# Optimization experiments

Hardware: AMD Instinct MI355X
Metric: run time of the kernel (lower is better)

The kernel has to match this reference:

```python
import jax, jax.numpy as jnp
import numpy as np

D_MODEL = 1024
N_HEADS = 16
HEAD_DIM = D_MODEL // N_HEADS
D_FF = 4096
B, T = 2, 2048


def layernorm(x, g, b, eps=1e-5):
    mu = jnp.mean(x, axis=-1, keepdims=True)
    var = jnp.var(x, axis=-1, keepdims=True)
    return (x - mu) * jax.lax.rsqrt(var + eps) * g + b


def setup_inputs() -> dict:
    key = jax.random.key(0)
    ks = jax.random.split(key, 8)
    s = 0.02
    return {
        "x": jax.random.normal(ks[0], (B, T, D_MODEL), dtype=jnp.float32),
        "ln1_g": jnp.ones((D_MODEL,), jnp.float32),
        "ln1_b": jnp.zeros((D_MODEL,), jnp.float32),
        "qkv_w": jax.random.normal(ks[1], (D_MODEL, 3 * D_MODEL), jnp.float32) * s,
        "qkv_b": jnp.zeros((3 * D_MODEL,), jnp.float32),
        "proj_w": jax.random.normal(ks[2], (D_MODEL, D_MODEL), jnp.float32) * s,
        "proj_b": jnp.zeros((D_MODEL,), jnp.float32),
        "ln2_g": jnp.ones((D_MODEL,), jnp.float32),
        "ln2_b": jnp.zeros((D_MODEL,), jnp.float32),
        "mlp_w1": jax.random.normal(ks[3], (D_MODEL, D_FF), jnp.float32) * s,
        "mlp_b1": jnp.zeros((D_FF,), jnp.float32),
        "mlp_w2": jax.random.normal(ks[4], (D_FF, D_MODEL), jnp.float32) * s,
        "mlp_b2": jnp.zeros((D_MODEL,), jnp.float32),
    }


def reference(x, ln1_g, ln1_b, qkv_w, qkv_b, proj_w, proj_b,
              ln2_g, ln2_b, mlp_w1, mlp_b1, mlp_w2, mlp_b2):
    Bv, Tv, C = x.shape
    scale = HEAD_DIM ** -0.5
    # --- attention branch ---
    h = layernorm(x, ln1_g, ln1_b)
    qkv = h @ qkv_w + qkv_b                                   # [B,T,3C]
    qkv = qkv.reshape(Bv, Tv, 3, N_HEADS, HEAD_DIM)
    q, k, v = qkv[:, :, 0], qkv[:, :, 1], qkv[:, :, 2]        # [B,T,H,Dh]
    att = jnp.einsum('bqhd,bkhd->bhqk', q, k) * scale         # [B,H,T,T]
    causal = jnp.tril(jnp.ones((Tv, Tv), dtype=bool))
    att = jnp.where(causal[None, None], att, -jnp.inf)
    att = jax.nn.softmax(att, axis=-1)
    out = jnp.einsum('bhqk,bkhd->bqhd', att, v).reshape(Bv, Tv, C)
    out = out @ proj_w + proj_b
    x = x + out
    # --- mlp branch ---
    h2 = layernorm(x, ln2_g, ln2_b)
    h2 = jax.nn.gelu(h2 @ mlp_w1 + mlp_b1, approximate=False)
    x = x + (h2 @ mlp_w2 + mlp_b2)
    return x
```

## Files before the change

kernel.cpp:

```cpp
#include <hip/hip_runtime.h>
#include <hip/hip_bf16.h>
#include <cstdint>

typedef __attribute__((ext_vector_type(4))) float f32x4;
typedef __attribute__((ext_vector_type(16))) float f32x16;
typedef __attribute__((ext_vector_type(8))) __bf16 bf16x8;
typedef __attribute__((ext_vector_type(4))) __bf16 bf16x4;
typedef __attribute__((ext_vector_type(4))) uint32_t u32x4;
typedef __attribute__((ext_vector_type(2))) unsigned int u32x2;

#define EPI_BF16 0
#define EPI_GELU 1
#define EPI_RES  2
#define EPI_PART 3

__device__ __forceinline__ void gll16(const void* g, void* l) {
  __builtin_amdgcn_global_load_lds((__attribute__((address_space(1))) void*)(g),
                                   (__attribute__((address_space(3))) void*)(l), 16, 0, 0);
}

__global__ __launch_bounds__(256)
void convT(const float* __restrict__ W, __bf16* __restrict__ WT, int Kd, int Nd)
{
  __shared__ __bf16 t[64][72];
  const int tid = threadIdx.x;
  const int n0 = blockIdx.x * 64, k0 = blockIdx.y * 64;
#pragma unroll
  for (int i = 0; i < 4; ++i) {
    const int c = i * 256 + tid;
    const int r = c >> 4, cc = (c & 15) * 4;
    const float4 v = *(const float4*)(W + (size_t)(k0 + r) * Nd + n0 + cc);
    bf16x4 tv; tv[0] = (__bf16)v.x; tv[1] = (__bf16)v.y; tv[2] = (__bf16)v.z; tv[3] = (__bf16)v.w;
    *(bf16x4*)&t[r][cc] = tv;
  }
  __syncthreads();
#pragma unroll
  for (int i = 0; i < 2; ++i) {
    const int c = i * 256 + tid;
    const int n = c >> 3, s = (c & 7) * 8;
    bf16x8 o;
#pragma unroll
    for (int j = 0; j < 8; ++j) o[j] = t[s + j][n];
    *(bf16x8*)(WT + (size_t)(n0 + n) * Kd + k0 + s) = o;
  }
}

__global__ __launch_bounds__(256)
void ln_rows(const float* __restrict__ x, const float* __restrict__ g,
             const float* __restrict__ b, __bf16* __restrict__ out)
{
  const int row = blockIdx.x;
  const int tid = threadIdx.x;
  const float4 v = *(const float4*)(x + (size_t)row * 1024 + tid * 4);
  float s = v.x + v.y + v.z + v.w;
  float q = v.x * v.x + v.y * v.y + v.z * v.z + v.w * v.w;
#pragma unroll
  for (int o = 32; o; o >>= 1) { s += __shfl_xor(s, o); q += __shfl_xor(q, o); }
  __shared__ float red[8];
  const int wid = tid >> 6;
  if ((tid & 63) == 0) { red[wid] = s; red[4 + wid] = q; }
  __syncthreads();
  s = red[0] + red[1] + red[2] + red[3];
  q = red[4] + red[5] + red[6] + red[7];
  const float mu = s * (1.0f / 1024.0f);
  const float var = q * (1.0f / 1024.0f) - mu * mu;
  const float rs = rsqrtf(var + 1e-5f);
  bf16x4 o4;
#pragma unroll
  for (int i = 0; i < 4; ++i) {
    const int c = tid * 4 + i;
    const float xv = (&v.x)[i];
    o4[i] = (__bf16)((xv - mu) * rs * g[c] + b[c]);
  }
  *(bf16x4*)(out + (size_t)row * 1024 + tid * 4) = o4;
}

template<int EPI>
__global__ __launch_bounds__(256)
void gemm_bt(const __bf16* __restrict__ A, const __bf16* __restrict__ BT,
             const float* __restrict__ bias, const float* __restrict__ R,
             void* __restrict__ Out, int M, int N, int K)
{
  const int tid = threadIdx.x;
  const int lane = tid & 63, wid = tid >> 6;
  const int l15 = lane & 15, lg = lane >> 4;
  const int wm = (wid >> 1) * 64, wn = (wid & 1) * 64;
  const int nwg = gridDim.x * gridDim.y;
  const int hw = blockIdx.y * gridDim.x + blockIdx.x;
  const int logical = (hw & 7) * (nwg >> 3) + (hw >> 3);
  const int rowBase = (logical / gridDim.x) * 128;
  const int colBase = (logical % gridDim.x) * 128;
  const int kLen = K / gridDim.z;
  const int kBeg = blockIdx.z * kLen;
  __shared__ __bf16 As[128 * 32];
  __shared__ __bf16 Bs[128 * 32];
  f32x4 acc[4][4] = {};
  const int fsw = ((l15 >> 1) & 3) << 3;

  for (int k0 = kBeg; k0 < kBeg + kLen; k0 += 32) {
#pragma unroll
    for (int i = 0; i < 2; ++i) {
      const int c = i * 256 + tid;
      const int r = c >> 2;
      const int s = ((c & 3) ^ ((r >> 1) & 3)) * 8;
      gll16(A + (size_t)(rowBase + r) * K + (k0 + s), As + c * 8);
    }
#pragma unroll
    for (int i = 0; i < 2; ++i) {
      const int c = i * 256 + tid;
      const int r = c >> 2;
      const int s = ((c & 3) ^ ((r >> 1) & 3)) * 8;
      gll16(BT + (size_t)(colBase + r) * K + (k0 + s), Bs + c * 8);
    }
    __syncthreads();
    bf16x8 af[4], bfr[4];
#pragma unroll
    for (int m = 0; m < 4; ++m) af[m] = *(const bf16x8*)(As + (wm + m * 16 + l15) * 32 + (lg * 8 ^ fsw));
#pragma unroll
    for (int n = 0; n < 4; ++n) bfr[n] = *(const bf16x8*)(Bs + (wn + n * 16 + l15) * 32 + (lg * 8 ^ fsw));
#pragma unroll
    for (int m = 0; m < 4; ++m)
#pragma unroll
      for (int n = 0; n < 4; ++n)
        acc[m][n] = __builtin_amdgcn_mfma_f32_16x16x32_bf16(af[m], bfr[n], acc[m][n], 0, 0, 0);
    __syncthreads();
  }
#pragma unroll
  for (int m = 0; m < 4; ++m) {
#pragma unroll
    for (int n = 0; n < 4; ++n) {
      const int col = colBase + wn + n * 16 + l15;
      float bb = 0.0f;
      if constexpr (EPI != EPI_PART) bb = bias[col];
#pragma unroll
      for (int i = 0; i < 4; ++i) {
        const int row = rowBase + wm + m * 16 + lg * 4 + i;
        float v = acc[m][n][i] + bb;
        if constexpr (EPI == EPI_GELU) {
          v = 0.5f * v * (1.0f + erff(v * 0.70710678118654752f));
          ((__bf16*)Out)[(size_t)row * N + col] = (__bf16)v;
        } else if constexpr (EPI == EPI_BF16) {
          ((__bf16*)Out)[(size_t)row * N + col] = (__bf16)v;
        } else if constexpr (EPI == EPI_RES) {
          v += R[(size_t)row * N + col];
          ((float*)Out)[(size_t)row * N + col] = v;
        } else {
          ((float*)Out)[((size_t)blockIdx.z * M + row) * N + col] = v;
        }
      }
    }
  }
}

__global__ __launch_bounds__(256)
void reduce2(const float* __restrict__ P, const float* __restrict__ bias,
             const float* __restrict__ R, float* __restrict__ Out, int MN, int N)
{
  const size_t e = ((size_t)blockIdx.x * 256 + threadIdx.x) * 4;
  const float4 a = *(const float4*)(P + e);
  const float4 b = *(const float4*)(P + (size_t)MN + e);
  const float4 r = *(const float4*)(R + e);
  const float4 bb = *(const float4*)(bias + (e & (size_t)(N - 1)));
  float4 o;
  o.x = a.x + b.x + r.x + bb.x;
  o.y = a.y + b.y + r.y + bb.y;
  o.z = a.z + b.z + r.z + bb.z;
  o.w = a.w + b.w + r.w + bb.w;
  *(float4*)(Out + e) = o;
}

__global__ __launch_bounds__(256)
void rearrange(const __bf16* __restrict__ qkv, __bf16* __restrict__ Q,
               __bf16* __restrict__ Kb, __bf16* __restrict__ VT)
{
  __shared__ __bf16 vt[64][72];
  const int tid = threadIdx.x;
  const int bid = blockIdx.x;
  const int bh = bid >> 5, tt = bid & 31;
  const int b = bh >> 4, h = bh & 15;
  const int t0 = tt * 64;
#pragma unroll
  for (int i = 0; i < 2; ++i) {
    const int c = i * 256 + tid;
    const int tk = c >> 3, d0 = (c & 7) * 8;
    const size_t srow = (size_t)(b * 2048 + t0 + tk) * 3072 + h * 64 + d0;
    const size_t drow = (size_t)(bh * 2048 + t0 + tk) * 64 + d0;
    *(bf16x8*)(Q + drow) = *(const bf16x8*)(qkv + srow);
    *(bf16x8*)(Kb + drow) = *(const bf16x8*)(qkv + srow + 1024);
    *(bf16x8*)&vt[tk][d0] = *(const bf16x8*)(qkv + srow + 2048);
  }
  __syncthreads();
#pragma unroll
  for (int i = 0; i < 2; ++i) {
    const int c = i * 256 + tid;
    const int d = c >> 3, s = (c & 7) * 8;
    bf16x8 o;
#pragma unroll
    for (int j = 0; j < 8; ++j) o[j] = vt[s + j][d];
    *(bf16x8*)(VT + (size_t)(bh * 64 + d) * 2048 + t0 + s) = o;
  }
}

__global__ __launch_bounds__(128)
void attn(const __bf16* __restrict__ Q, const __bf16* __restrict__ K,
          const __bf16* __restrict__ VT, __bf16* __restrict__ O)
{
  const int bid = blockIdx.x;
  const int bh = bid >> 5, qt = 31 - (bid & 31);
  const int tid = threadIdx.x;
  const int lane = tid & 63, w = tid >> 6;
  const int l31 = lane & 31, hi = lane >> 5;
  __shared__ __bf16 Ks[64 * 64];
  __shared__ __bf16 Vs[64 * 64];
  const size_t base = (size_t)bh * 2048 * 64;
  const int qrow0 = qt * 64 + w * 32;
  const int xsw = (l31 & 7) << 3;

  bf16x8 qf[4];
#pragma unroll
  for (int s = 0; s < 4; ++s)
    qf[s] = *(const bf16x8*)(Q + base + (size_t)(qrow0 + l31) * 64 + s * 16 + hi * 8);

  f32x16 oa0 = {}, oa1 = {};
  float mst = -INFINITY, lst = 0.0f;

  for (int j = 0; j <= qt; ++j) {
#pragma unroll
    for (int rnd = 0; rnd < 4; ++rnd) {
      const int c = rnd * 128 + tid;
      const int r = c >> 3;
      const int e = ((c & 7) ^ (r & 7)) * 8;
      gll16(K + base + (size_t)(j * 64 + r) * 64 + e, Ks + c * 8);
      gll16(VT + base + (size_t)r * 2048 + j * 64 + e, Vs + c * 8);
    }
    __syncthreads();

    f32x16 s0v = {}, s1v = {};
#pragma unroll
    for (int s = 0; s < 4; ++s) {
      const int co = (s * 16 + hi * 8) ^ xsw;
      bf16x8 ak0 = *(const bf16x8*)(Ks + l31 * 64 + co);
      bf16x8 ak1 = *(const bf16x8*)(Ks + (32 + l31) * 64 + co);
      s0v = __builtin_amdgcn_mfma_f32_32x32x16_bf16(ak0, qf[s], s0v, 0, 0, 0);
      s1v = __builtin_amdgcn_mfma_f32_32x32x16_bf16(ak1, qf[s], s1v, 0, 0, 0);
    }
#pragma unroll
    for (int rg = 0; rg < 16; ++rg) { s0v[rg] *= 0.125f; s1v[rg] *= 0.125f; }
    if (j == qt) {
      const int qg = qrow0 + l31;
#pragma unroll
      for (int rg = 0; rg < 16; ++rg) {
        const int kr = j * 64 + ((rg & 3) + 8 * (rg >> 2)) + 4 * hi;
        if (kr > qg) s0v[rg] = -INFINITY;
        if (kr + 32 > qg) s1v[rg] = -INFINITY;
      }
    }
    float mx = s0v[0];
#pragma unroll
    for (int rg = 1; rg < 16; ++rg) mx = fmaxf(mx, s0v[rg]);
#pragma unroll
    for (int rg = 0; rg < 16; ++rg) mx = fmaxf(mx, s1v[rg]);
    mx = fmaxf(mx, __shfl_xor(mx, 32));
    const float mnew = fmaxf(mst, mx);
    const float cf = __expf(mst - mnew);
    float rs = 0.0f;
#pragma unroll
    for (int rg = 0; rg < 16; ++rg) {
      s0v[rg] = __expf(s0v[rg] - mnew); rs += s0v[rg];
      s1v[rg] = __expf(s1v[rg] - mnew); rs += s1v[rg];
    }
    rs += __shfl_xor(rs, 32);
    lst = lst * cf + rs;
    mst = mnew;
#pragma unroll
    for (int rg = 0; rg < 16; ++rg) {
      const float cb = __shfl(cf, (rg & 3) + 8 * (rg >> 2) + 4 * hi);
      oa0[rg] *= cb; oa1[rg] *= cb;
    }
#pragma unroll
    for (int s = 0; s < 4; ++s) {
      const int br = (s & 1) * 8;
      uint32_t wA0, wA1, wB0, wB1;
      if (s < 2) {
        asm("v_cvt_pk_bf16_f32 %0, %1, %2" : "=v"(wA0) : "v"(s0v[br + 0]), "v"(s0v[br + 1]));
        asm("v_cvt_pk_bf16_f32 %0, %1, %2" : "=v"(wA1) : "v"(s0v[br + 2]), "v"(s0v[br + 3]));
        asm("v_cvt_pk_bf16_f32 %0, %1, %2" : "=v"(wB0) : "v"(s0v[br + 4]), "v"(s0v[br + 5]));
        asm("v_cvt_pk_bf16_f32 %0, %1, %2" : "=v"(wB1) : "v"(s0v[br + 6]), "v"(s0v[br + 7]));
      } else {
        asm("v_cvt_pk_bf16_f32 %0, %1, %2" : "=v"(wA0) : "v"(s1v[br + 0]), "v"(s1v[br + 1]));
        asm("v_cvt_pk_bf16_f32 %0, %1, %2" : "=v"(wA1) : "v"(s1v[br + 2]), "v"(s1v[br + 3]));
        asm("v_cvt_pk_bf16_f32 %0, %1, %2" : "=v"(wB0) : "v"(s1v[br + 4]), "v"(s1v[br + 5]));
        asm("v_cvt_pk_bf16_f32 %0, %1, %2" : "=v"(wB1) : "v"(s1v[br + 6]), "v"(s1v[br + 7]));
      }
      const u32x2 r0 = __builtin_amdgcn_permlane32_swap(wA0, wB0, false, false);
      const u32x2 r1 = __builtin_amdgcn_permlane32_swap(wA1, wB1, false, false);
      u32x4 uu; uu.x = r0.x; uu.y = r1.x; uu.z = r0.y; uu.w = r1.y;
      const bf16x8 pa = __builtin_bit_cast(bf16x8, uu);
      const int co = (s * 16 + hi * 8) ^ xsw;
      bf16x8 bv0 = *(const bf16x8*)(Vs + l31 * 64 + co);
      bf16x8 bv1 = *(const bf16x8*)(Vs + (32 + l31) * 64 + co);
      oa0 = __builtin_amdgcn_mfma_f32_32x32x16_bf16(pa, bv0, oa0, 0, 0, 0);
      oa1 = __builtin_amdgcn_mfma_f32_32x32x16_bf16(pa, bv1, oa1, 0, 0, 0);
    }
    __syncthreads();
  }
  const float inv = 1.0f / lst;
  const int b = bh >> 4, hd = bh & 15;
#pragma unroll
  for (int rg = 0; rg < 16; ++rg) {
    const int cr = (rg & 3) + 8 * (rg >> 2) + 4 * hi;
    const float ib = __shfl(inv, cr);
    const int qr = qrow0 + cr;
    O[(size_t)(b * 2048 + qr) * 1024 + hd * 64 + l31]      = (__bf16)(oa0[rg] * ib);
    O[(size_t)(b * 2048 + qr) * 1024 + hd * 64 + 32 + l31] = (__bf16)(oa1[rg] * ib);
  }
}

extern "C" void kernel_launch(void* const* d_in, const int* in_sizes, int n_in,
                              void* d_out, int out_size, void* d_ws, size_t ws_size,
                              hipStream_t stream)
{
  const float* x      = (const float*)d_in[0];
  const float* ln1_g  = (const float*)d_in[1];
  const float* ln1_b  = (const float*)d_in[2];
  const float* qkv_w  = (const float*)d_in[3];
  const float* qkv_b  = (const float*)d_in[4];
  const float* proj_w = (const float*)d_in[5];
  const float* proj_b = (const float*)d_in[6];
  const float* ln2_g  = (const float*)d_in[7];
  const float* ln2_b  = (const float*)d_in[8];
  const float* mlp_w1 = (const float*)d_in[9];
  const float* mlp_b1 = (const float*)d_in[10];
  const float* mlp_w2 = (const float*)d_in[11];
  const float* mlp_b2 = (const float*)d_in[12];

  char* ws = (char*)d_ws;
  __bf16* qkvT  = (__bf16*)(ws + 0);
  __bf16* projT = (__bf16*)(ws + 6291456);
  __bf16* w1T   = (__bf16*)(ws + 8388608);
  __bf16* w2T   = (__bf16*)(ws + 16777216);
  float*  x2    = (float*) (ws + 25165824);
  __bf16* act1  = (__bf16*)(ws + 41943040);
  __bf16* h1    = (__bf16*)(ws + 41943040);
  __bf16* qkv   = (__bf16*)(ws + 50331648);
  float*  part  = (float*) (ws + 75497472);
  __bf16* h2    = (__bf16*)(ws + 75497472);
  __bf16* Qb    = (__bf16*)(ws + 75497472);
  __bf16* Kb    = (__bf16*)(ws + 83886080);
  __bf16* VTb   = (__bf16*)(ws + 92274688);
  __bf16* attO  = (__bf16*)(ws + 100663296);

  convT<<<dim3(48, 16), 256, 0, stream>>>(qkv_w, qkvT, 1024, 3072);
  convT<<<dim3(16, 16), 256, 0, stream>>>(proj_w, projT, 1024, 1024);
  convT<<<dim3(64, 16), 256, 0, stream>>>(mlp_w1, w1T, 1024, 4096);
  convT<<<dim3(16, 64), 256, 0, stream>>>(mlp_w2, w2T, 4096, 1024);

  ln_rows<<<4096, 256, 0, stream>>>(x, ln1_g, ln1_b, h1);
  gemm_bt<EPI_BF16><<<dim3(24, 32), 256, 0, stream>>>(h1, qkvT, qkv_b, nullptr, qkv, 4096, 3072, 1024);
  rearrange<<<1024, 256, 0, stream>>>(qkv, Qb, Kb, VTb);
  attn<<<1024, 128, 0, stream>>>(Qb, Kb, VTb, attO);
  gemm_bt<EPI_RES><<<dim3(8, 32), 256, 0, stream>>>(attO, projT, proj_b, x, x2, 4096, 1024, 1024);
  ln_rows<<<4096, 256, 0, stream>>>(x2, ln2_g, ln2_b, h2);
  gemm_bt<EPI_GELU><<<dim3(32, 32), 256, 0, stream>>>(h2, w1T, mlp_b1, nullptr, act1, 4096, 4096, 1024);
  gemm_bt<EPI_PART><<<dim3(8, 32, 2), 256, 0, stream>>>(act1, w2T, nullptr, nullptr, part, 4096, 1024, 4096);
  reduce2<<<4096, 256, 0, stream>>>(part, mlp_b2, x2, (float*)d_out, 4096 * 1024, 1024);
}
```

Measured before the change: 417.6 us.

## Merge weight conversions, split-K proj GEMM, 4-way bf16 split-K for MLP down-proj

Fuses the four weight transpose/convert launches into one kernel that dispatches on block index. The attention output projection becomes a 2-way split-K GEMM with a separate reduce that adds bias and residual. The MLP down-projection moves from 2-way fp32 partials to 4-way bf16 partials reduced by a new kernel. The aim is more blocks in flight for the small-N GEMMs (256 blocks before) and fewer launches, at the cost of extra partial-sum traffic, extra reduce launches, and bf16 rounding of the partial sums.

```diff
diff --git a/kernel.cpp b/kernel.cpp
--- a/kernel.cpp
+++ b/kernel.cpp
@@ -9,10 +9,11 @@
 typedef __attribute__((ext_vector_type(4))) uint32_t u32x4;
 typedef __attribute__((ext_vector_type(2))) unsigned int u32x2;
 
-#define EPI_BF16 0
-#define EPI_GELU 1
-#define EPI_RES  2
-#define EPI_PART 3
+#define EPI_BF16  0
+#define EPI_GELU  1
+#define EPI_RES   2
+#define EPI_PART  3
+#define EPI_PARTB 4
 
 __device__ __forceinline__ void gll16(const void* g, void* l) {
   __builtin_amdgcn_global_load_lds((__attribute__((address_space(1))) void*)(g),
@@ -20,11 +21,20 @@
 }
 
 __global__ __launch_bounds__(256)
-void convT(const float* __restrict__ W, __bf16* __restrict__ WT, int Kd, int Nd)
+void convT_all(const float* __restrict__ W0, __bf16* __restrict__ T0,
+               const float* __restrict__ W1, __bf16* __restrict__ T1,
+               const float* __restrict__ W2, __bf16* __restrict__ T2,
+               const float* __restrict__ W3, __bf16* __restrict__ T3)
 {
   __shared__ __bf16 t[64][72];
+  const int bid = blockIdx.x;
+  const float* W; __bf16* WT; int Kd, Nd, nx, lb;
+  if (bid < 768)       { W = W0; WT = T0; Kd = 1024; Nd = 3072; nx = 48; lb = bid; }
+  else if (bid < 1024) { W = W1; WT = T1; Kd = 1024; Nd = 1024; nx = 16; lb = bid - 768; }
+  else if (bid < 2048) { W = W2; WT = T2; Kd = 1024; Nd = 4096; nx = 64; lb = bid - 1024; }
+  else                 { W = W3; WT = T3; Kd = 4096; Nd = 1024; nx = 16; lb = bid - 2048; }
   const int tid = threadIdx.x;
-  const int n0 = blockIdx.x * 64, k0 = blockIdx.y * 64;
+  const int n0 = (lb % nx) * 64, k0 = (lb / nx) * 64;
 #pragma unroll
   for (int i = 0; i < 4; ++i) {
     const int c = i * 256 + tid;
@@ -131,7 +141,7 @@
     for (int n = 0; n < 4; ++n) {
       const int col = colBase + wn + n * 16 + l15;
       float bb = 0.0f;
-      if constexpr (EPI != EPI_PART) bb = bias[col];
+      if constexpr (EPI != EPI_PART && EPI != EPI_PARTB) bb = bias[col];
 #pragma unroll
       for (int i = 0; i < 4; ++i) {
         const int row = rowBase + wm + m * 16 + lg * 4 + i;
@@ -144,8 +154,10 @@
         } else if constexpr (EPI == EPI_RES) {
           v += R[(size_t)row * N + col];
           ((float*)Out)[(size_t)row * N + col] = v;
+        } else if constexpr (EPI == EPI_PART) {
+          ((float*)Out)[((size_t)blockIdx.z * M + row) * N + col] = v;
         } else {
-          ((float*)Out)[((size_t)blockIdx.z * M + row) * N + col] = v;
+          ((__bf16*)Out)[((size_t)blockIdx.z * M + row) * N + col] = (__bf16)v;
         }
       }
     }
@@ -167,6 +179,32 @@
   o.z = a.z + b.z + r.z + bb.z;
   o.w = a.w + b.w + r.w + bb.w;
   *(float4*)(Out + e) = o;
+}
+
+__global__ __launch_bounds__(256)
+void reduce4(const __bf16* __restrict__ P, const float* __restrict__ bias,
+             const float* __restrict__ R, float* __restrict__ Out, int MN, int N)
+{
+  const size_t e = ((size_t)blockIdx.x * 256 + threadIdx.x) * 8;
+  float s[8];
+#pragma unroll
+  for (int i = 0; i < 8; ++i) s[i] = 0.0f;
+#pragma unroll
+  for (int p = 0; p < 4; ++p) {
+    const bf16x8 v = *(const bf16x8*)(P + (size_t)p * MN + e);
+#pragma unroll
+    for (int i = 0; i < 8; ++i) s[i] += (float)v[i];
+  }
+  const size_t col = e & (size_t)(N - 1);
+  const float4 r0 = *(const float4*)(R + e),       r1 = *(const float4*)(R + e + 4);
+  const float4 b0 = *(const float4*)(bias + col),  b1 = *(const float4*)(bias + col + 4);
+  float4 o0, o1;
+  o0.x = s[0] + r0.x + b0.x; o0.y = s[1] + r0.y + b0.y;
+  o0.z = s[2] + r0.z + b0.z; o0.w = s[3] + r0.w + b0.w;
+  o1.x = s[4] + r1.x + b1.x; o1.y = s[5] + r1.y + b1.y;
+  o1.z = s[6] + r1.z + b1.z; o1.w = s[7] + r1.w + b1.w;
+  *(float4*)(Out + e)     = o0;
+  *(float4*)(Out + e + 4) = o1;
 }
 
 __global__ __launch_bounds__(256)
@@ -340,28 +378,27 @@
   __bf16* w1T   = (__bf16*)(ws + 8388608);
   __bf16* w2T   = (__bf16*)(ws + 16777216);
   float*  x2    = (float*) (ws + 25165824);
-  __bf16* act1  = (__bf16*)(ws + 41943040);
   __bf16* h1    = (__bf16*)(ws + 41943040);
+  float*  partP = (float*) (ws + 41943040);
+  __bf16* part2 = (__bf16*)(ws + 41943040);
   __bf16* qkv   = (__bf16*)(ws + 50331648);
-  float*  part  = (float*) (ws + 75497472);
+  __bf16* Qb    = (__bf16*)(ws + 75497472);
   __bf16* h2    = (__bf16*)(ws + 75497472);
-  __bf16* Qb    = (__bf16*)(ws + 75497472);
   __bf16* Kb    = (__bf16*)(ws + 83886080);
+  __bf16* act1  = (__bf16*)(ws + 83886080);
   __bf16* VTb   = (__bf16*)(ws + 92274688);
   __bf16* attO  = (__bf16*)(ws + 100663296);
 
-  convT<<<dim3(48, 16), 256, 0, stream>>>(qkv_w, qkvT, 1024, 3072);
-  convT<<<dim3(16, 16), 256, 0, stream>>>(proj_w, projT, 1024, 1024);
-  convT<<<dim3(64, 16), 256, 0, stream>>>(mlp_w1, w1T, 1024, 4096);
-  convT<<<dim3(16, 64), 256, 0, stream>>>(mlp_w2, w2T, 4096, 1024);
+  convT_all<<<3072, 256, 0, stream>>>(qkv_w, qkvT, proj_w, projT, mlp_w1, w1T, mlp_w2, w2T);
 
   ln_rows<<<4096, 256, 0, stream>>>(x, ln1_g, ln1_b, h1);
   gemm_bt<EPI_BF16><<<dim3(24, 32), 256, 0, stream>>>(h1, qkvT, qkv_b, nullptr, qkv, 4096, 3072, 1024);
   rearrange<<<1024, 256, 0, stream>>>(qkv, Qb, Kb, VTb);
   attn<<<1024, 128, 0, stream>>>(Qb, Kb, VTb, attO);
-  gemm_bt<EPI_RES><<<dim3(8, 32), 256, 0, stream>>>(attO, projT, proj_b, x, x2, 4096, 1024, 1024);
+  gemm_bt<EPI_PART><<<dim3(8, 32, 2), 256, 0, stream>>>(attO, projT, nullptr, nullptr, partP, 4096, 1024, 1024);
+  reduce2<<<4096, 256, 0, stream>>>(partP, proj_b, x, x2, 4096 * 1024, 1024);
   ln_rows<<<4096, 256, 0, stream>>>(x2, ln2_g, ln2_b, h2);
   gemm_bt<EPI_GELU><<<dim3(32, 32), 256, 0, stream>>>(h2, w1T, mlp_b1, nullptr, act1, 4096, 4096, 1024);
-  gemm_bt<EPI_PART><<<dim3(8, 32, 2), 256, 0, stream>>>(act1, w2T, nullptr, nullptr, part, 4096, 1024, 4096);
-  reduce2<<<4096, 256, 0, stream>>>(part, mlp_b2, x2, (float*)d_out, 4096 * 1024, 1024);
-}
+  gemm_bt<EPI_PARTB><<<dim3(8, 32, 4), 256, 0, stream>>>(act1, w2T, nullptr, nullptr, part2, 4096, 1024, 4096);
+  reduce4<<<2048, 256, 0, stream>>>(part2, mlp_b2, x2, (float*)d_out, 4096 * 1024, 1024);
+}
```

After: 414.9 us. No clear change (-0.7%).
